# Kernel tuning notes

Measured on AMD Instinct MI355X. Metric: run time of the kernel, lower is better.

The kernel has to match this reference:

```python
import jax, jax.numpy as jnp
import numpy as np

HEAD_NUM = 8
EMB_SIZE = 768
B, N = 8, 1024


def setup_inputs() -> dict:
    key = jax.random.key(0)
    ks = jax.random.split(key, 9)
    s = 0.02
    return {
        "x": jax.random.normal(ks[0], (B, N, EMB_SIZE), dtype=jnp.float32),
        "Wq": jax.random.normal(ks[1], (EMB_SIZE, EMB_SIZE), dtype=jnp.float32) * s,
        "bq": jax.random.normal(ks[2], (EMB_SIZE,), dtype=jnp.float32) * s,
        "Wk": jax.random.normal(ks[3], (EMB_SIZE, EMB_SIZE), dtype=jnp.float32) * s,
        "bk": jax.random.normal(ks[4], (EMB_SIZE,), dtype=jnp.float32) * s,
        "Wv": jax.random.normal(ks[5], (EMB_SIZE, EMB_SIZE), dtype=jnp.float32) * s,
        "bv": jax.random.normal(ks[6], (EMB_SIZE,), dtype=jnp.float32) * s,
        "Wp": jax.random.normal(ks[7], (EMB_SIZE, EMB_SIZE), dtype=jnp.float32) * s,
        "bp": jax.random.normal(ks[8], (EMB_SIZE,), dtype=jnp.float32) * s,
    }


def reference(x, Wq, bq, Wk, bk, Wv, bv, Wp, bp):
    b, n, e = x.shape
    h = HEAD_NUM
    d = e // h
    # nn.Linear: y = x @ W^T + b
    q = (x @ Wq.T + bq).reshape(b, h, n, d)  # NOTE: raw reshape, as in source
    k = (x @ Wk.T + bk).reshape(b, h, n, d)
    v = (x @ Wv.T + bv).reshape(b, h, n, d)
    energy = jnp.einsum('bhqd,bhkd->bhqk', q, k)
    # source divides by sqrt(emb_size) AFTER softmax (faithful)
    attn = jax.nn.softmax(energy, axis=-1) / jnp.sqrt(jnp.float32(e))
    out = jnp.einsum('bhql,bhld->bhqd', attn, v).reshape(b, n, h * d)
    return out @ Wp.T + bp
```

## Files before the change

### kernel.cpp

```cpp
#include <hip/hip_runtime.h>
#include <hip/hip_bf16.h>


typedef __attribute__((ext_vector_type(8))) short short8;
typedef __attribute__((ext_vector_type(4))) float floatx4;
typedef __attribute__((ext_vector_type(16))) float floatx16;

static constexpr int EMB = 768;
static constexpr int SEQ = 1024;
static constexpr int DH = 96;
static constexpr int NBH = 64;
static constexpr int HEADBLK = SEQ * DH;
static constexpr int MROWS = 8192;
static constexpr int NW = EMB * EMB;
static constexpr int QKVN = 3 * EMB;

__device__ __forceinline__ unsigned bfround(float f) {
    unsigned u = __builtin_bit_cast(unsigned, f);
    return u + 0x7FFFu + ((u >> 16) & 1u);
}
__device__ __forceinline__ unsigned short f2bf(float f) {
    return (unsigned short)(bfround(f) >> 16);
}
__device__ __forceinline__ unsigned pk2(float lo, float hi) {
    return (bfround(lo) >> 16) | (bfround(hi) & 0xFFFF0000u);
}

__device__ __forceinline__ void gload16(const unsigned short* g, unsigned short* l) {
    __builtin_amdgcn_global_load_lds(
        (const __attribute__((address_space(1))) unsigned int*)g,
        (__attribute__((address_space(3))) unsigned int*)l, 16, 0, 0);
}

__global__ void cast_all(const float* __restrict__ x,
                         const float* __restrict__ Wq, const float* __restrict__ Wk,
                         const float* __restrict__ Wv, const float* __restrict__ Wp,
                         const float* __restrict__ bq, const float* __restrict__ bk,
                         const float* __restrict__ bv,
                         unsigned short* __restrict__ xb,
                         unsigned short* __restrict__ Wqkv, unsigned short* __restrict__ Wpb,
                         float* __restrict__ bias) {
    int bx = blockIdx.x;
    if (bx < 6144) {
        int i = bx * 1024 + threadIdx.x * 4;
        float4 v = *reinterpret_cast<const float4*>(x + i);
        ushort4 o;
        o.x = f2bf(v.x); o.y = f2bf(v.y); o.z = f2bf(v.z); o.w = f2bf(v.w);
        *reinterpret_cast<ushort4*>(xb + i) = o;
    } else if (bx < 8448) {
        int i4 = (bx - 6144) * 1024 + threadIdx.x * 4;
        const float* src;
        unsigned short* dst;
        if (i4 < 3 * NW) {
            int wi = i4 / NW;
            src = (wi == 0) ? Wq + i4 : (wi == 1) ? Wk + (i4 - NW) : Wv + (i4 - 2 * NW);
            dst = Wqkv + i4;
        } else {
            src = Wp + (i4 - 3 * NW);
            dst = Wpb + (i4 - 3 * NW);
        }
        float4 v = *reinterpret_cast<const float4*>(src);
        ushort4 o;
        o.x = f2bf(v.x); o.y = f2bf(v.y); o.z = f2bf(v.z); o.w = f2bf(v.w);
        *reinterpret_cast<ushort4*>(dst) = o;
    } else {
        int j = (bx - 8448) * 256 + threadIdx.x;
        if (j < QKVN)
            bias[j] = (j < 768) ? bq[j] : (j < 1536) ? bk[j - 768] : bv[j - 1536];
    }
}

__global__ __launch_bounds__(256) void gemm_qkv(
    const unsigned short* __restrict__ A,
    const unsigned short* __restrict__ Bm,
    const float* __restrict__ bias,
    unsigned short* __restrict__ Qo,
    unsigned short* __restrict__ Ko,
    unsigned short* __restrict__ Vo) {
    __shared__ unsigned short As[128 * 64];
    __shared__ unsigned short Bs[128 * 64];
    const int K = EMB;

    const int t = threadIdx.x;
    const int lane = t & 63;
    const int w = t >> 6;
    const int wm = (w >> 1) * 64;
    const int wn = (w & 1) * 64;
    const int l32 = lane & 31;
    const int lh = lane >> 5;
    const int bm = blockIdx.x * 128;
    const int by = blockIdx.y;
    const int bn = by * 128;

    const unsigned short* Agp[4];
    const unsigned short* Bgp[4];
#pragma unroll
    for (int i = 0; i < 4; i++) {
        int f = i * 2048 + w * 512 + lane * 8;
        int row = f >> 6;
        int cc = (f >> 3) & 7;
        int gk = (cc ^ (row & 7)) * 8;
        Agp[i] = A + (size_t)(bm + row) * K + gk;
        Bgp[i] = Bm + (size_t)(bn + row) * K + gk;
    }

    floatx16 acc[2][2];
#pragma unroll
    for (int i = 0; i < 2; i++)
#pragma unroll
        for (int j = 0; j < 2; j++)
#pragma unroll
            for (int r = 0; r < 16; r++) acc[i][j][r] = 0.0f;

    const int sx = lane & 7;
    for (int k0 = 0; k0 < K; k0 += 64) {
        __syncthreads();
#pragma unroll
        for (int i = 0; i < 4; i++) {
            gload16(Agp[i] + k0, As + i * 2048 + w * 512);
            gload16(Bgp[i] + k0, Bs + i * 2048 + w * 512);
        }
        __syncthreads();

#pragma unroll
        for (int ks = 0; ks < 4; ks++) {
            const int co = ((ks * 2 + lh) ^ sx) * 8;
            short8 af[2], bfr[2];
#pragma unroll
            for (int mt = 0; mt < 2; mt++)
                af[mt] = *reinterpret_cast<const short8*>(As + (wm + mt * 32 + l32) * 64 + co);
#pragma unroll
            for (int nt = 0; nt < 2; nt++)
                bfr[nt] = *reinterpret_cast<const short8*>(Bs + (wn + nt * 32 + l32) * 64 + co);
#pragma unroll
            for (int mt = 0; mt < 2; mt++)
#pragma unroll
                for (int nt = 0; nt < 2; nt++)
                    acc[mt][nt] = __builtin_amdgcn_mfma_f32_32x32x16_bf16(af[mt], bfr[nt], acc[mt][nt], 0, 0, 0);
        }
    }

    unsigned short* dst = (by < 6) ? Qo : (by < 12) ? Ko : Vo;
    const int bnl = (by % 6) * 128;
#pragma unroll
    for (int mt = 0; mt < 2; mt++) {
#pragma unroll
        for (int nt = 0; nt < 2; nt++) {
            int colg = bn + wn + nt * 32 + l32;
            int coll = bnl + wn + nt * 32 + l32;
            float bb = bias[colg];
#pragma unroll
            for (int rg = 0; rg < 4; rg++) {
                int rowb = bm + wm + mt * 32 + rg * 8 + lh * 4;
#pragma unroll
                for (int rr = 0; rr < 4; rr++)
                    dst[(size_t)(rowb + rr) * EMB + coll] = f2bf(acc[mt][nt][rg * 4 + rr] + bb);
            }
        }
    }
}

__global__ __launch_bounds__(256) void gemm_proj(
    const unsigned short* __restrict__ A,
    const unsigned short* __restrict__ Bm,
    const float* __restrict__ bias,
    float* __restrict__ C) {
    __shared__ unsigned short As[64 * 64];
    __shared__ unsigned short Bs[128 * 64];
    const int K = EMB, N = EMB;

    const int t = threadIdx.x;
    const int lane = t & 63;
    const int w = t >> 6;
    const int wm = (w >> 1) * 32;
    const int wn = (w & 1) * 64;
    const int l32 = lane & 31;
    const int lh = lane >> 5;
    const int bm = blockIdx.x * 64;
    const int bn = blockIdx.y * 128;

    const unsigned short* Agp[2];
    const unsigned short* Bgp[4];
#pragma unroll
    for (int i = 0; i < 2; i++) {
        int f = i * 2048 + w * 512 + lane * 8;
        int row = f >> 6;
        int cc = (f >> 3) & 7;
        Agp[i] = A + (size_t)(bm + row) * K + ((cc ^ (row & 7)) * 8);
    }
#pragma unroll
    for (int i = 0; i < 4; i++) {
        int f = i * 2048 + w * 512 + lane * 8;
        int row = f >> 6;
        int cc = (f >> 3) & 7;
        Bgp[i] = Bm + (size_t)(bn + row) * K + ((cc ^ (row & 7)) * 8);
    }

    floatx16 acc[2];
#pragma unroll
    for (int j = 0; j < 2; j++)
#pragma unroll
        for (int r = 0; r < 16; r++) acc[j][r] = 0.0f;

    const int sx = lane & 7;
    for (int k0 = 0; k0 < K; k0 += 64) {
        __syncthreads();
#pragma unroll
        for (int i = 0; i < 2; i++) gload16(Agp[i] + k0, As + i * 2048 + w * 512);
#pragma unroll
        for (int i = 0; i < 4; i++) gload16(Bgp[i] + k0, Bs + i * 2048 + w * 512);
        __syncthreads();

#pragma unroll
        for (int ks = 0; ks < 4; ks++) {
            const int co = ((ks * 2 + lh) ^ sx) * 8;
            short8 af = *reinterpret_cast<const short8*>(As + (wm + l32) * 64 + co);
            short8 bfr[2];
#pragma unroll
            for (int nt = 0; nt < 2; nt++)
                bfr[nt] = *reinterpret_cast<const short8*>(Bs + (wn + nt * 32 + l32) * 64 + co);
#pragma unroll
            for (int nt = 0; nt < 2; nt++)
                acc[nt] = __builtin_amdgcn_mfma_f32_32x32x16_bf16(af, bfr[nt], acc[nt], 0, 0, 0);
        }
    }

#pragma unroll
    for (int nt = 0; nt < 2; nt++) {
        int col = bn + wn + nt * 32 + l32;
        float bb = bias[col];
#pragma unroll
        for (int rg = 0; rg < 4; rg++) {
            int rowb = bm + wm + rg * 8 + lh * 4;
#pragma unroll
            for (int rr = 0; rr < 4; rr++)
                C[(size_t)(rowb + rr) * N + col] = acc[nt][rg * 4 + rr] + bb;
        }
    }
}

__global__ __launch_bounds__(256) void transpose_v(const unsigned short* __restrict__ V,
                                                   unsigned short* __restrict__ Vt) {
    __shared__ unsigned short L[64 * 104];
    const int t = threadIdx.x;
    const int bh = blockIdx.x, nb = blockIdx.y;
    const unsigned short* Vg = V + (size_t)bh * HEADBLK + (size_t)nb * 64 * DH;
#pragma unroll
    for (int i = 0; i < 3; i++) {
        int f = i * 2048 + t * 8;
        int r = f / 96, c = f - r * 96;
        *reinterpret_cast<short8*>(L + r * 104 + c) = *reinterpret_cast<const short8*>(Vg + f);
    }
    __syncthreads();
    unsigned short* dst = Vt + (size_t)bh * HEADBLK;
#pragma unroll
    for (int i = 0; i < 3; i++) {
        int f = i * 2048 + t * 8;
        int d = f >> 6, c0 = f & 63;
        union { short8 s; unsigned short u[8]; } o;
#pragma unroll
        for (int j = 0; j < 8; j++) {
            int c = c0 + j;
            int key = (c & ~12) | ((c & 4) << 1) | ((c & 8) >> 1);
            o.u[j] = L[key * 104 + d];
        }
        *reinterpret_cast<short8*>(dst + d * SEQ + nb * 64 + c0) = o.s;
    }
}

__global__ __launch_bounds__(256, 2) void attn_kernel(
    const unsigned short* __restrict__ Q,
    const unsigned short* __restrict__ K,
    const unsigned short* __restrict__ Vt,
    unsigned short* __restrict__ O) {
    __shared__ unsigned short Ks[2 * 64 * 104];
    __shared__ unsigned short Vs[2 * 96 * 72];
    const int KSZ = 64 * 104;
    const int VSZ = 96 * 72;

    const int t = threadIdx.x;
    const int lane = t & 63;
    const int w = t >> 6;
    const int l32 = lane & 31;
    const int lh = lane >> 5;
    const int bh = blockIdx.x, qb = blockIdx.y;

    const unsigned short* Qh = Q + (size_t)bh * HEADBLK;
    const unsigned short* Kh = K + (size_t)bh * HEADBLK;
    const unsigned short* Vth = Vt + (size_t)bh * HEADBLK;

    short8 qf[6];
    {
        const unsigned short* qsrc = Qh + (size_t)(qb * 128 + w * 32 + l32) * DH + lh * 8;
#pragma unroll
        for (int ks = 0; ks < 6; ks++)
            qf[ks] = *reinterpret_cast<const short8*>(qsrc + ks * 16);
    }

    const unsigned short* Kp[3];
    const unsigned short* Vp[3];
    unsigned short* KsW[3];
    unsigned short* VsW[3];
#pragma unroll
    for (int i = 0; i < 3; i++) {
        int f = i * 2048 + t * 8;
        int r = f / 96, c = f - r * 96;
        Kp[i] = Kh + f;
        KsW[i] = Ks + r * 104 + c;
        int d = f >> 6, cv = f & 63;
        Vp[i] = Vth + d * SEQ + cv;
        VsW[i] = Vs + d * 72 + cv;
    }

    short8 kreg[3], vreg[3];
#pragma unroll
    for (int i = 0; i < 3; i++) {
        kreg[i] = *reinterpret_cast<const short8*>(Kp[i]);
        vreg[i] = *reinterpret_cast<const short8*>(Vp[i]);
    }

    float l_ = 0.0f;
    floatx16 acco[3];
#pragma unroll
    for (int n = 0; n < 3; n++)
#pragma unroll
        for (int r = 0; r < 16; r++) acco[n][r] = 0.0f;

    for (int kb = 0; kb < 16; kb++) {
        const int ko = (kb & 1) * KSZ;
        const int vo = (kb & 1) * VSZ;
#pragma unroll
        for (int i = 0; i < 3; i++) {
            *reinterpret_cast<short8*>(KsW[i] + ko) = kreg[i];
            *reinterpret_cast<short8*>(VsW[i] + vo) = vreg[i];
        }
        if (kb < 15) {
#pragma unroll
            for (int i = 0; i < 3; i++) {
                kreg[i] = *reinterpret_cast<const short8*>(Kp[i] + (kb + 1) * 6144);
                vreg[i] = *reinterpret_cast<const short8*>(Vp[i] + (kb + 1) * 64);
            }
        }
        asm volatile("s_waitcnt lgkmcnt(0)" ::: "memory");
        __builtin_amdgcn_s_barrier();

        floatx16 sacc[2];
#pragma unroll
        for (int kt = 0; kt < 2; kt++)
#pragma unroll
            for (int r = 0; r < 16; r++) sacc[kt][r] = 0.0f;

#pragma unroll
        for (int ks = 0; ks < 6; ks++) {
#pragma unroll
            for (int kt = 0; kt < 2; kt++) {
                short8 ak = *reinterpret_cast<const short8*>(
                    Ks + ko + (kt * 32 + l32) * 104 + ks * 16 + lh * 8);
                sacc[kt] = __builtin_amdgcn_mfma_f32_32x32x16_bf16(ak, qf[ks], sacc[kt], 0, 0, 0);
            }
        }

        float rs = 0.0f;
#pragma unroll
        for (int kt = 0; kt < 2; kt++)
#pragma unroll
            for (int r = 0; r < 16; r++) {
                float v = __expf(sacc[kt][r]);
                sacc[kt][r] = v;
                rs += v;
            }
        rs += __shfl_xor(rs, 32);
        l_ += rs;

#pragma unroll
        for (int kt2 = 0; kt2 < 4; kt2++) {
            const int kt = kt2 >> 1, ro = (kt2 & 1) * 8;
            union { short8 s8; unsigned u[4]; } bp;
#pragma unroll
            for (int p = 0; p < 4; p++)
                bp.u[p] = pk2(sacc[kt][ro + 2 * p], sacc[kt][ro + 2 * p + 1]);
#pragma unroll
            for (int n = 0; n < 3; n++) {
                short8 av = *reinterpret_cast<const short8*>(
                    Vs + vo + (n * 32 + l32) * 72 + kt2 * 16 + lh * 8);
                acco[n] = __builtin_amdgcn_mfma_f32_32x32x16_bf16(av, bp.s8, acco[n], 0, 0, 0);
            }
        }
    }

    const float inv_sqrt_e = 0.036084391824351615f;
    float invl = inv_sqrt_e / l_;
    unsigned short* dst = O + (size_t)bh * HEADBLK +
                          (size_t)(qb * 128 + w * 32 + l32) * DH + lh * 4;
#pragma unroll
    for (int n = 0; n < 3; n++) {
#pragma unroll
        for (int rg = 0; rg < 4; rg++) {
            uint2 o2;
            o2.x = pk2(acco[n][rg * 4 + 0] * invl, acco[n][rg * 4 + 1] * invl);
            o2.y = pk2(acco[n][rg * 4 + 2] * invl, acco[n][rg * 4 + 3] * invl);
            *reinterpret_cast<uint2*>(dst + n * 32 + rg * 8) = o2;
        }
    }
}

extern "C" void kernel_launch(void* const* d_in, const int* in_sizes, int n_in,
                              void* d_out, int out_size, void* d_ws, size_t ws_size,
                              hipStream_t stream) {
    const float* x = (const float*)d_in[0];
    const float* Wq = (const float*)d_in[1];
    const float* bq = (const float*)d_in[2];
    const float* Wk = (const float*)d_in[3];
    const float* bk = (const float*)d_in[4];
    const float* Wv = (const float*)d_in[5];
    const float* bv = (const float*)d_in[6];
    const float* Wp = (const float*)d_in[7];
    const float* bp = (const float*)d_in[8];
    float* out = (float*)d_out;

    char* ws = (char*)d_ws;
    size_t off = 0;
    auto alloc = [&](size_t bytes) {
        char* p = ws + off;
        off += (bytes + 255) & ~(size_t)255;
        return p;
    };
    const int nx = MROWS * EMB;
    unsigned short* xb    = (unsigned short*)alloc((size_t)nx * 2);
    unsigned short* Wqkvb = (unsigned short*)alloc((size_t)3 * NW * 2);
    unsigned short* Wpb   = (unsigned short*)alloc((size_t)NW * 2);
    float*          biasq = (float*)alloc((size_t)QKVN * 4);
    unsigned short* Qb    = (unsigned short*)alloc((size_t)nx * 2);
    unsigned short* Kb    = (unsigned short*)alloc((size_t)nx * 2);
    unsigned short* Vb    = (unsigned short*)alloc((size_t)nx * 2);
    unsigned short* Vtb   = (unsigned short*)alloc((size_t)nx * 2);
    unsigned short* Ob    = (unsigned short*)alloc((size_t)nx * 2);

    cast_all<<<8457, 256, 0, stream>>>(x, Wq, Wk, Wv, Wp, bq, bk, bv,
                                       xb, Wqkvb, Wpb, biasq);

    gemm_qkv<<<dim3(MROWS / 128, QKVN / 128), 256, 0, stream>>>(
        xb, Wqkvb, biasq, Qb, Kb, Vb);

    transpose_v<<<dim3(NBH, SEQ / 64), 256, 0, stream>>>(Vb, Vtb);

    attn_kernel<<<dim3(NBH, SEQ / 128), 256, 0, stream>>>(Qb, Kb, Vtb, Ob);

    gemm_proj<<<dim3(MROWS / 64, EMB / 128), 256, 0, stream>>>(Ob, Wpb, bp, out);
}
```

Baseline: 191.7 us.

## Software-pipeline attention loop to overlap next QK^T with softmax and PV

Restructures the attention key-block loop so the QK^T MFMAs for block kb+1 are issued before the exp/row-sum and PV MFMAs of block kb. Two score accumulators alternate, and V staging is delayed one step to match. This lets matrix-core work overlap with the transcendental/VALU softmax work. In exchange it keeps a second 32-float score accumulator live, which raises register pressure and may cut occupancy.

```diff
diff --git a/kernel.cpp b/kernel.cpp
--- a/kernel.cpp
+++ b/kernel.cpp
@@ -326,67 +326,107 @@
 #pragma unroll
         for (int r = 0; r < 16; r++) acco[n][r] = 0.0f;
 
-    for (int kb = 0; kb < 16; kb++) {
-        const int ko = (kb & 1) * KSZ;
-        const int vo = (kb & 1) * VSZ;
-#pragma unroll
-        for (int i = 0; i < 3; i++) {
-            *reinterpret_cast<short8*>(KsW[i] + ko) = kreg[i];
-            *reinterpret_cast<short8*>(VsW[i] + vo) = vreg[i];
-        }
-        if (kb < 15) {
-#pragma unroll
-            for (int i = 0; i < 3; i++) {
-                kreg[i] = *reinterpret_cast<const short8*>(Kp[i] + (kb + 1) * 6144);
-                vreg[i] = *reinterpret_cast<const short8*>(Vp[i] + (kb + 1) * 64);
-            }
-        }
+    floatx16 sA[2], sB[2];
+
+    auto wV = [&](int vb) {
+#pragma unroll
+        for (int i = 0; i < 3; i++)
+            *reinterpret_cast<short8*>(VsW[i] + vb * VSZ) = vreg[i];
+    };
+    auto wK = [&](int kwb) {
+#pragma unroll
+        for (int i = 0; i < 3; i++)
+            *reinterpret_cast<short8*>(KsW[i] + kwb * KSZ) = kreg[i];
+    };
+    auto ldK = [&](int kb1) {
+#pragma unroll
+        for (int i = 0; i < 3; i++)
+            kreg[i] = *reinterpret_cast<const short8*>(Kp[i] + kb1 * 6144);
+    };
+    auto ldV = [&](int kb) {
+#pragma unroll
+        for (int i = 0; i < 3; i++)
+            vreg[i] = *reinterpret_cast<const short8*>(Vp[i] + kb * 64);
+    };
+    auto fence = [&]() {
         asm volatile("s_waitcnt lgkmcnt(0)" ::: "memory");
         __builtin_amdgcn_s_barrier();
-
-        floatx16 sacc[2];
+    };
+    auto qk = [&](floatx16 (&cur)[2], int kwb) {
 #pragma unroll
         for (int kt = 0; kt < 2; kt++)
 #pragma unroll
-            for (int r = 0; r < 16; r++) sacc[kt][r] = 0.0f;
-
-#pragma unroll
-        for (int ks = 0; ks < 6; ks++) {
+            for (int r = 0; r < 16; r++) cur[kt][r] = 0.0f;
+#pragma unroll
+        for (int ks = 0; ks < 6; ks++)
 #pragma unroll
             for (int kt = 0; kt < 2; kt++) {
                 short8 ak = *reinterpret_cast<const short8*>(
-                    Ks + ko + (kt * 32 + l32) * 104 + ks * 16 + lh * 8);
-                sacc[kt] = __builtin_amdgcn_mfma_f32_32x32x16_bf16(ak, qf[ks], sacc[kt], 0, 0, 0);
+                    Ks + kwb * KSZ + (kt * 32 + l32) * 104 + ks * 16 + lh * 8);
+                cur[kt] = __builtin_amdgcn_mfma_f32_32x32x16_bf16(ak, qf[ks], cur[kt], 0, 0, 0);
             }
-        }
-
+    };
+    auto sm = [&](floatx16 (&prv)[2]) {
         float rs = 0.0f;
 #pragma unroll
         for (int kt = 0; kt < 2; kt++)
 #pragma unroll
             for (int r = 0; r < 16; r++) {
-                float v = __expf(sacc[kt][r]);
-                sacc[kt][r] = v;
+                float v = __expf(prv[kt][r]);
+                prv[kt][r] = v;
                 rs += v;
             }
         rs += __shfl_xor(rs, 32);
         l_ += rs;
-
+    };
+    auto pv = [&](floatx16 (&prv)[2], int vb) {
 #pragma unroll
         for (int kt2 = 0; kt2 < 4; kt2++) {
             const int kt = kt2 >> 1, ro = (kt2 & 1) * 8;
             union { short8 s8; unsigned u[4]; } bp;
 #pragma unroll
             for (int p = 0; p < 4; p++)
-                bp.u[p] = pk2(sacc[kt][ro + 2 * p], sacc[kt][ro + 2 * p + 1]);
+                bp.u[p] = pk2(prv[kt][ro + 2 * p], prv[kt][ro + 2 * p + 1]);
 #pragma unroll
             for (int n = 0; n < 3; n++) {
                 short8 av = *reinterpret_cast<const short8*>(
-                    Vs + vo + (n * 32 + l32) * 72 + kt2 * 16 + lh * 8);
+                    Vs + vb * VSZ + (n * 32 + l32) * 72 + kt2 * 16 + lh * 8);
                 acco[n] = __builtin_amdgcn_mfma_f32_32x32x16_bf16(av, bp.s8, acco[n], 0, 0, 0);
             }
         }
-    }
+    };
+
+    wK(0);
+    ldK(1);
+    fence();
+    qk(sA, 0);
+
+    for (int kb = 1; kb <= 13; kb += 2) {
+        wV((kb - 1) & 1); wK(kb & 1);
+        ldK(kb + 1); ldV(kb);
+        fence();
+        qk(sB, kb & 1);
+        sm(sA);
+        pv(sA, (kb - 1) & 1);
+        wV(kb & 1); wK((kb + 1) & 1);
+        ldK(kb + 2); ldV(kb + 1);
+        fence();
+        qk(sA, (kb + 1) & 1);
+        sm(sB);
+        pv(sB, kb & 1);
+    }
+
+    wV(0); wK(1);
+    ldV(15);
+    fence();
+    qk(sB, 1);
+    sm(sA);
+    pv(sA, 0);
+
+    wV(1);
+    fence();
+    sm(sB);
+    pv(sB, 1);
 
     const float inv_sqrt_e = 0.036084391824351615f;
     float invl = inv_sqrt_e / l_;
```

Result: no change. 191.8 us (+0.0%).

## Fuse all stages into one persistent cooperative kernel with grid syncs

Applied to the files above, without the earlier changes.

Replaces the five separate launches (cast, QKV GEMM, V transpose, attention, projection) with one cooperative persistent kernel of 512 blocks. Each stage loops over its tiles and the stages are separated by grid-wide syncs. This is meant to remove launch gaps and tail effects between kernels. In exchange, fixed launch bounds and a shared LDS size limit occupancy, and uneven tile counts per stage can leave blocks idle at each grid sync. If the cooperative launch fails, the code falls back to the original five launches.

```diff
diff --git a/kernel.cpp b/kernel.cpp
--- a/kernel.cpp
+++ b/kernel.cpp
@@ -1,5 +1,8 @@
 #include <hip/hip_runtime.h>
 #include <hip/hip_bf16.h>
+#include <hip/hip_cooperative_groups.h>
+
+namespace cg = cooperative_groups;
 
 
 typedef __attribute__((ext_vector_type(8))) short short8;
@@ -30,6 +33,371 @@
     __builtin_amdgcn_global_load_lds(
         (const __attribute__((address_space(1))) unsigned int*)g,
         (__attribute__((address_space(3))) unsigned int*)l, 16, 0, 0);
+}
+
+__global__ __launch_bounds__(256, 2) void mha_fused(
+    const float* __restrict__ x,
+    const float* __restrict__ Wq, const float* __restrict__ bq,
+    const float* __restrict__ Wk, const float* __restrict__ bk,
+    const float* __restrict__ Wv, const float* __restrict__ bv,
+    const float* __restrict__ Wp, const float* __restrict__ bp,
+    unsigned short* __restrict__ xb, unsigned short* __restrict__ Wqkvb,
+    unsigned short* __restrict__ Wpb, float* __restrict__ biasq,
+    unsigned short* __restrict__ Qb, unsigned short* __restrict__ Kb,
+    unsigned short* __restrict__ Vb, unsigned short* __restrict__ Vtb,
+    unsigned short* __restrict__ Ob, float* __restrict__ out) {
+    __shared__ __align__(16) char shmem[54272];
+    cg::grid_group gg = cg::this_grid();
+
+    const int t = threadIdx.x;
+    const int lane = t & 63;
+    const int w = t >> 6;
+    const int l32 = lane & 31;
+    const int lh = lane >> 5;
+    const int sx = lane & 7;
+    const int NB = gridDim.x;
+
+    for (int bx = blockIdx.x; bx < 8457; bx += NB) {
+        if (bx < 6144) {
+            int i = bx * 1024 + t * 4;
+            float4 v = *reinterpret_cast<const float4*>(x + i);
+            ushort4 o;
+            o.x = f2bf(v.x); o.y = f2bf(v.y); o.z = f2bf(v.z); o.w = f2bf(v.w);
+            *reinterpret_cast<ushort4*>(xb + i) = o;
+        } else if (bx < 8448) {
+            int i4 = (bx - 6144) * 1024 + t * 4;
+            const float* src;
+            unsigned short* dst;
+            if (i4 < 3 * NW) {
+                int wi = i4 / NW;
+                src = (wi == 0) ? Wq + i4 : (wi == 1) ? Wk + (i4 - NW) : Wv + (i4 - 2 * NW);
+                dst = Wqkvb + i4;
+            } else {
+                src = Wp + (i4 - 3 * NW);
+                dst = Wpb + (i4 - 3 * NW);
+            }
+            float4 v = *reinterpret_cast<const float4*>(src);
+            ushort4 o;
+            o.x = f2bf(v.x); o.y = f2bf(v.y); o.z = f2bf(v.z); o.w = f2bf(v.w);
+            *reinterpret_cast<ushort4*>(dst) = o;
+        } else {
+            int j = (bx - 8448) * 256 + t;
+            if (j < QKVN)
+                biasq[j] = (j < 768) ? bq[j] : (j < 1536) ? bk[j - 768] : bv[j - 1536];
+        }
+    }
+    gg.sync();
+
+    {
+        unsigned short* As = (unsigned short*)shmem;
+        unsigned short* Bs = As + 128 * 64;
+        for (int tile = blockIdx.x; tile < 1152; tile += NB) {
+            const int bm = (tile & 63) * 128;
+            const int by = tile >> 6;
+            const int bn = by * 128;
+
+            const unsigned short* Agp[4];
+            const unsigned short* Bgp[4];
+#pragma unroll
+            for (int i = 0; i < 4; i++) {
+                int f = i * 2048 + w * 512 + lane * 8;
+                int row = f >> 6;
+                int cc = (f >> 3) & 7;
+                int gk = (cc ^ (row & 7)) * 8;
+                Agp[i] = xb + (size_t)(bm + row) * EMB + gk;
+                Bgp[i] = Wqkvb + (size_t)(bn + row) * EMB + gk;
+            }
+            const int wm = (w >> 1) * 64;
+            const int wn = (w & 1) * 64;
+
+            floatx16 acc[2][2];
+#pragma unroll
+            for (int i = 0; i < 2; i++)
+#pragma unroll
+                for (int j = 0; j < 2; j++)
+#pragma unroll
+                    for (int r = 0; r < 16; r++) acc[i][j][r] = 0.0f;
+
+            for (int k0 = 0; k0 < EMB; k0 += 64) {
+                __syncthreads();
+#pragma unroll
+                for (int i = 0; i < 4; i++) {
+                    gload16(Agp[i] + k0, As + i * 2048 + w * 512);
+                    gload16(Bgp[i] + k0, Bs + i * 2048 + w * 512);
+                }
+                __syncthreads();
+
+#pragma unroll
+                for (int ks = 0; ks < 4; ks++) {
+                    const int co = ((ks * 2 + lh) ^ sx) * 8;
+                    short8 af[2], bfr[2];
+#pragma unroll
+                    for (int mt = 0; mt < 2; mt++)
+                        af[mt] = *reinterpret_cast<const short8*>(As + (wm + mt * 32 + l32) * 64 + co);
+#pragma unroll
+                    for (int nt = 0; nt < 2; nt++)
+                        bfr[nt] = *reinterpret_cast<const short8*>(Bs + (wn + nt * 32 + l32) * 64 + co);
+#pragma unroll
+                    for (int mt = 0; mt < 2; mt++)
+#pragma unroll
+                        for (int nt = 0; nt < 2; nt++)
+                            acc[mt][nt] = __builtin_amdgcn_mfma_f32_32x32x16_bf16(
+                                af[mt], bfr[nt], acc[mt][nt], 0, 0, 0);
+                }
+            }
+            __syncthreads();
+
+            unsigned short* dst = (by < 6) ? Qb : (by < 12) ? Kb : Vb;
+            const int bnl = (by % 6) * 128;
+#pragma unroll
+            for (int mt = 0; mt < 2; mt++) {
+#pragma unroll
+                for (int nt = 0; nt < 2; nt++) {
+                    int colg = bn + wn + nt * 32 + l32;
+                    int coll = bnl + wn + nt * 32 + l32;
+                    float bb = biasq[colg];
+#pragma unroll
+                    for (int rg = 0; rg < 4; rg++) {
+                        int rowb = bm + wm + mt * 32 + rg * 8 + lh * 4;
+#pragma unroll
+                        for (int rr = 0; rr < 4; rr++)
+                            dst[(size_t)(rowb + rr) * EMB + coll] = f2bf(acc[mt][nt][rg * 4 + rr] + bb);
+                    }
+                }
+            }
+        }
+    }
+    gg.sync();
+
+    {
+        unsigned short* L = (unsigned short*)shmem;
+        for (int tile = blockIdx.x; tile < 1024; tile += NB) {
+            __syncthreads();
+            const int bh = tile & 63, nb = tile >> 6;
+            const unsigned short* Vg = Vb + (size_t)bh * HEADBLK + (size_t)nb * 64 * DH;
+#pragma unroll
+            for (int i = 0; i < 3; i++) {
+                int f = i * 2048 + t * 8;
+                int r = f / 96, c = f - r * 96;
+                *reinterpret_cast<short8*>(L + r * 104 + c) = *reinterpret_cast<const short8*>(Vg + f);
+            }
+            __syncthreads();
+            unsigned short* dstv = Vtb + (size_t)bh * HEADBLK;
+#pragma unroll
+            for (int i = 0; i < 3; i++) {
+                int f = i * 2048 + t * 8;
+                int d = f >> 6, c0 = f & 63;
+                union { short8 s; unsigned short u[8]; } o;
+#pragma unroll
+                for (int j = 0; j < 8; j++) {
+                    int c = c0 + j;
+                    int key = (c & ~12) | ((c & 4) << 1) | ((c & 8) >> 1);
+                    o.u[j] = L[key * 104 + d];
+                }
+                *reinterpret_cast<short8*>(dstv + d * SEQ + nb * 64 + c0) = o.s;
+            }
+        }
+    }
+    gg.sync();
+
+    {
+        unsigned short* Ks = (unsigned short*)shmem;
+        unsigned short* Vs = Ks + 2 * 64 * 104;
+        const int KSZ = 64 * 104;
+        const int VSZ = 96 * 72;
+
+        unsigned short* KsW[3];
+        unsigned short* VsW[3];
+        int kfo[3], vfo[3];
+#pragma unroll
+        for (int i = 0; i < 3; i++) {
+            int f = i * 2048 + t * 8;
+            int r = f / 96, c = f - r * 96;
+            kfo[i] = f;
+            KsW[i] = Ks + r * 104 + c;
+            int d = f >> 6, cv = f & 63;
+            vfo[i] = d * SEQ + cv;
+            VsW[i] = Vs + d * 72 + cv;
+        }
+
+        for (int tile = blockIdx.x; tile < 512; tile += NB) {
+            __syncthreads();
+            const int bh = tile & 63, qb = tile >> 6;
+            const unsigned short* Qh = Qb + (size_t)bh * HEADBLK;
+            const unsigned short* Kh = Kb + (size_t)bh * HEADBLK;
+            const unsigned short* Vth = Vtb + (size_t)bh * HEADBLK;
+
+            short8 qf[6];
+            {
+                const unsigned short* qsrc = Qh + (size_t)(qb * 128 + w * 32 + l32) * DH + lh * 8;
+#pragma unroll
+                for (int ks = 0; ks < 6; ks++)
+                    qf[ks] = *reinterpret_cast<const short8*>(qsrc + ks * 16);
+            }
+
+            short8 kreg[3], vreg[3];
+#pragma unroll
+            for (int i = 0; i < 3; i++) {
+                kreg[i] = *reinterpret_cast<const short8*>(Kh + kfo[i]);
+                vreg[i] = *reinterpret_cast<const short8*>(Vth + vfo[i]);
+            }
+
+            float l_ = 0.0f;
+            floatx16 acco[3];
+#pragma unroll
+            for (int n = 0; n < 3; n++)
+#pragma unroll
+                for (int r = 0; r < 16; r++) acco[n][r] = 0.0f;
+
+            for (int kb = 0; kb < 16; kb++) {
+                const int ko = (kb & 1) * KSZ;
+                const int vo = (kb & 1) * VSZ;
+#pragma unroll
+                for (int i = 0; i < 3; i++) {
+                    *reinterpret_cast<short8*>(KsW[i] + ko) = kreg[i];
+                    *reinterpret_cast<short8*>(VsW[i] + vo) = vreg[i];
+                }
+                if (kb < 15) {
+#pragma unroll
+                    for (int i = 0; i < 3; i++) {
+                        kreg[i] = *reinterpret_cast<const short8*>(Kh + kfo[i] + (kb + 1) * 6144);
+                        vreg[i] = *reinterpret_cast<const short8*>(Vth + vfo[i] + (kb + 1) * 64);
+                    }
+                }
+                asm volatile("s_waitcnt lgkmcnt(0)" ::: "memory");
+                __builtin_amdgcn_s_barrier();
+
+                floatx16 sacc[2];
+#pragma unroll
+                for (int kt = 0; kt < 2; kt++)
+#pragma unroll
+                    for (int r = 0; r < 16; r++) sacc[kt][r] = 0.0f;
+
+#pragma unroll
+                for (int ks = 0; ks < 6; ks++) {
+#pragma unroll
+                    for (int kt = 0; kt < 2; kt++) {
+                        short8 ak = *reinterpret_cast<const short8*>(
+                            Ks + ko + (kt * 32 + l32) * 104 + ks * 16 + lh * 8);
+                        sacc[kt] = __builtin_amdgcn_mfma_f32_32x32x16_bf16(ak, qf[ks], sacc[kt], 0, 0, 0);
+                    }
+                }
+
+                float rs = 0.0f;
+#pragma unroll
+                for (int kt = 0; kt < 2; kt++)
+#pragma unroll
+                    for (int r = 0; r < 16; r++) {
+                        float v = __expf(sacc[kt][r]);
+                        sacc[kt][r] = v;
+                        rs += v;
+                    }
+                rs += __shfl_xor(rs, 32);
+                l_ += rs;
+
+#pragma unroll
+                for (int kt2 = 0; kt2 < 4; kt2++) {
+                    const int kt = kt2 >> 1, ro = (kt2 & 1) * 8;
+                    union { short8 s8; unsigned u[4]; } bpk;
+#pragma unroll
+                    for (int p = 0; p < 4; p++)
+                        bpk.u[p] = pk2(sacc[kt][ro + 2 * p], sacc[kt][ro + 2 * p + 1]);
+#pragma unroll
+                    for (int n = 0; n < 3; n++) {
+                        short8 av = *reinterpret_cast<const short8*>(
+                            Vs + vo + (n * 32 + l32) * 72 + kt2 * 16 + lh * 8);
+                        acco[n] = __builtin_amdgcn_mfma_f32_32x32x16_bf16(av, bpk.s8, acco[n], 0, 0, 0);
+                    }
+                }
+            }
+
+            const float inv_sqrt_e = 0.036084391824351615f;
+            float invl = inv_sqrt_e / l_;
+            unsigned short* dsto = Ob + (size_t)bh * HEADBLK +
+                                   (size_t)(qb * 128 + w * 32 + l32) * DH + lh * 4;
+#pragma unroll
+            for (int n = 0; n < 3; n++) {
+#pragma unroll
+                for (int rg = 0; rg < 4; rg++) {
+                    uint2 o2;
+                    o2.x = pk2(acco[n][rg * 4 + 0] * invl, acco[n][rg * 4 + 1] * invl);
+                    o2.y = pk2(acco[n][rg * 4 + 2] * invl, acco[n][rg * 4 + 3] * invl);
+                    *reinterpret_cast<uint2*>(dsto + n * 32 + rg * 8) = o2;
+                }
+            }
+        }
+    }
+    gg.sync();
+
+    {
+        unsigned short* As = (unsigned short*)shmem;
+        unsigned short* Bs = As + 64 * 64;
+        for (int tile = blockIdx.x; tile < 768; tile += NB) {
+            const int bm = (tile & 127) * 64;
+            const int bn = (tile >> 7) * 128;
+            const int wm = (w >> 1) * 32;
+            const int wn = (w & 1) * 64;
+
+            const unsigned short* Agp[2];
+            const unsigned short* Bgp[4];
+#pragma unroll
+            for (int i = 0; i < 2; i++) {
+                int f = i * 2048 + w * 512 + lane * 8;
+                int row = f >> 6;
+                int cc = (f >> 3) & 7;
+                Agp[i] = Ob + (size_t)(bm + row) * EMB + ((cc ^ (row & 7)) * 8);
+            }
+#pragma unroll
+            for (int i = 0; i < 4; i++) {
+                int f = i * 2048 + w * 512 + lane * 8;
+                int row = f >> 6;
+                int cc = (f >> 3) & 7;
+                Bgp[i] = Wpb + (size_t)(bn + row) * EMB + ((cc ^ (row & 7)) * 8);
+            }
+
+            floatx16 acc[2];
+#pragma unroll
+            for (int j = 0; j < 2; j++)
+#pragma unroll
+                for (int r = 0; r < 16; r++) acc[j][r] = 0.0f;
+
+            for (int k0 = 0; k0 < EMB; k0 += 64) {
+                __syncthreads();
+#pragma unroll
+                for (int i = 0; i < 2; i++) gload16(Agp[i] + k0, As + i * 2048 + w * 512);
+#pragma unroll
+                for (int i = 0; i < 4; i++) gload16(Bgp[i] + k0, Bs + i * 2048 + w * 512);
+                __syncthreads();
+
+#pragma unroll
+                for (int ks = 0; ks < 4; ks++) {
+                    const int co = ((ks * 2 + lh) ^ sx) * 8;
+                    short8 af = *reinterpret_cast<const short8*>(As + (wm + l32) * 64 + co);
+                    short8 bfr[2];
+#pragma unroll
+                    for (int nt = 0; nt < 2; nt++)
+                        bfr[nt] = *reinterpret_cast<const short8*>(Bs + (wn + nt * 32 + l32) * 64 + co);
+#pragma unroll
+                    for (int nt = 0; nt < 2; nt++)
+                        acc[nt] = __builtin_amdgcn_mfma_f32_32x32x16_bf16(af, bfr[nt], acc[nt], 0, 0, 0);
+                }
+            }
+            __syncthreads();
+
+#pragma unroll
+            for (int nt = 0; nt < 2; nt++) {
+                int col = bn + wn + nt * 32 + l32;
+                float bb = bp[col];
+#pragma unroll
+                for (int rg = 0; rg < 4; rg++) {
+                    int rowb = bm + wm + rg * 8 + lh * 4;
+#pragma unroll
+                    for (int rr = 0; rr < 4; rr++)
+                        out[(size_t)(rowb + rr) * EMB + col] = acc[nt][rg * 4 + rr] + bb;
+                }
+            }
+        }
+    }
 }
 
 __global__ void cast_all(const float* __restrict__ x,
@@ -436,15 +804,23 @@
     unsigned short* Vtb   = (unsigned short*)alloc((size_t)nx * 2);
     unsigned short* Ob    = (unsigned short*)alloc((size_t)nx * 2);
 
-    cast_all<<<8457, 256, 0, stream>>>(x, Wq, Wk, Wv, Wp, bq, bk, bv,
-                                       xb, Wqkvb, Wpb, biasq);
-
-    gemm_qkv<<<dim3(MROWS / 128, QKVN / 128), 256, 0, stream>>>(
-        xb, Wqkvb, biasq, Qb, Kb, Vb);
-
-    transpose_v<<<dim3(NBH, SEQ / 64), 256, 0, stream>>>(Vb, Vtb);
-
-    attn_kernel<<<dim3(NBH, SEQ / 128), 256, 0, stream>>>(Qb, Kb, Vtb, Ob);
-
-    gemm_proj<<<dim3(MROWS / 64, EMB / 128), 256, 0, stream>>>(Ob, Wpb, bp, out);
-}
+    void* args[] = {
+        (void*)&x, (void*)&Wq, (void*)&bq, (void*)&Wk, (void*)&bk,
+        (void*)&Wv, (void*)&bv, (void*)&Wp, (void*)&bp,
+        (void*)&xb, (void*)&Wqkvb, (void*)&Wpb, (void*)&biasq,
+        (void*)&Qb, (void*)&Kb, (void*)&Vb, (void*)&Vtb, (void*)&Ob, (void*)&out
+    };
+
+    hipError_t err = hipLaunchCooperativeKernel(
+        (const void*)mha_fused, dim3(512), dim3(256), args, 0, stream);
+
+    if (err != hipSuccess) {
+        cast_all<<<8457, 256, 0, stream>>>(x, Wq, Wk, Wv, Wp, bq, bk, bv,
+                                           xb, Wqkvb, Wpb, biasq);
+        gemm_qkv<<<dim3(MROWS / 128, QKVN / 128), 256, 0, stream>>>(
+            xb, Wqkvb, biasq, Qb, Kb, Vb);
+        transpose_v<<<dim3(NBH, SEQ / 64), 256, 0, stream>>>(Vb, Vtb);
+        attn_kernel<<<dim3(NBH, SEQ / 128), 256, 0, stream>>>(Qb, Kb, Vtb, Ob);
+        gemm_proj<<<dim3(MROWS / 64, EMB / 128), 256, 0, stream>>>(Ob, Wpb, bp, out);
+    }
+}
```

After: 482.1 us. 151% more time.
